# Performance work log

Hardware: AMD Instinct MI355X
Metric: run time of the kernel (lower is better)

## Reference

```python
import jax, jax.numpy as jnp
import numpy as np

B, S, E, H = 2, 2048, 1024, 16
HD = E // H
DFF = 4 * E
LN_EPS = 1e-5


def _layernorm(x, g, b):
    mu = jnp.mean(x, axis=-1, keepdims=True)
    var = jnp.mean(jnp.square(x - mu), axis=-1, keepdims=True)
    return (x - mu) * jax.lax.rsqrt(var + LN_EPS) * g + b


def setup_inputs() -> dict:
    key = jax.random.key(0)
    ks = jax.random.split(key, 6)
    inp = {
        "x": jax.random.normal(ks[0], (B, S, E), jnp.float32),
        "ln1_g": jnp.ones((E,), jnp.float32),
        "ln1_b": jnp.zeros((E,), jnp.float32),
        "ln2_g": jnp.ones((E,), jnp.float32),
        "ln2_b": jnp.zeros((E,), jnp.float32),
        # OptimizedPoincareBallLinear init: randn * 0.1, zero bias
        "w_qkv": jax.random.normal(ks[1], (3 * E, E), jnp.float32) * 0.1,
        "b_qkv": jnp.zeros((3 * E,), jnp.float32),
        "w_ao": jax.random.normal(ks[2], (E, E), jnp.float32) * 0.1,
        "b_ao": jnp.zeros((E,), jnp.float32),
        "w_fc": jax.random.normal(ks[3], (DFF, E), jnp.float32) * 0.1,
        "b_fc": jnp.zeros((DFF,), jnp.float32),
        "w_po": jax.random.normal(ks[4], (E, DFF), jnp.float32) * 0.1,
        "b_po": jnp.zeros((E,), jnp.float32),
    }
    return inp


def reference(x, ln1_g, ln1_b, ln2_g, ln2_b, w_qkv, b_qkv, w_ao, b_ao,
              w_fc, b_fc, w_po, b_po):
    # --- attention branch ---
    h = _layernorm(x, ln1_g, ln1_b)
    qkv = h @ w_qkv.T + b_qkv                       # [B,S,3E]
    qkv = qkv.reshape(B, S, H, 3 * HD).transpose(0, 2, 1, 3)  # [B,H,S,3hd]
    q, k, v = jnp.split(qkv, 3, axis=-1)            # each [B,H,S,hd]
    scores = jnp.einsum('bhqd,bhkd->bhqk', q, k) / jnp.sqrt(
        jnp.asarray(HD, jnp.float32))
    causal = jnp.tril(jnp.ones((S, S), bool))        # attn_bias[:, :, :S, :S]
    scores = jnp.where(causal, scores, jnp.finfo(scores.dtype).min)
    attn_w = jax.nn.softmax(scores, axis=-1)         # dropout p=0.1 inactive (eval)
    attn = jnp.einsum('bhqk,bhkd->bhqd', attn_w, v)  # [B,H,S,hd]
    attn = attn.transpose(0, 2, 1, 3).reshape(B, S, E)
    attn = attn @ w_ao.T + b_ao
    x = x + attn
    # --- MLP branch ---
    h2 = _layernorm(x, ln2_g, ln2_b)
    h2 = h2 @ w_fc.T + b_fc
    h2 = jax.nn.gelu(h2, approximate=True)           # GPT-2 gelu_new
    h2 = h2 @ w_po.T + b_po
    x = x + h2
    return x
```

## Files before the change

kernel.cpp:

```cpp
#include <hip/hip_runtime.h>
#include <cstddef>
#include <cstdint>

#define Bc 2
#define Sc 2048
#define Ec 1024
#define Hc 16
#define HDc 64
#define DFFc 4096
#define ROWS (Bc * Sc)

typedef _Float16 half8v __attribute__((ext_vector_type(8)));
typedef _Float16 half4v __attribute__((ext_vector_type(4)));
typedef float f32x4 __attribute__((ext_vector_type(4)));
typedef _Float16 h16;

__device__ inline void gld_lds16(const void* g, void* l) {
    __builtin_amdgcn_global_load_lds(
        (const __attribute__((address_space(1))) void*)g,
        (__attribute__((address_space(3))) void*)l, 16, 0, 0);
}

__device__ inline float gelu_new(float x) {
    float x2 = x * x;
    float u = x * fmaf(0.07135481627362f, x2, 1.5957691216057308f);
    return x / (1.0f + __expf(-u));
}

__global__ __launch_bounds__(256) void cvt4_kernel(
    const float* __restrict__ a,
    const float* __restrict__ b,
    const float* __restrict__ c,
    const float* __restrict__ d,
    h16* __restrict__ out)
{
    int bid = blockIdx.x;
    const float* src;
    size_t obase;
    int base;
    if (bid < 3072)      { src = a; obase = 0;       base = bid; }
    else if (bid < 4096) { src = b; obase = 3145728; base = bid - 3072; }
    else if (bid < 8192) { src = c; obase = 4194304; base = bid - 4096; }
    else                 { src = d; obase = 8388608; base = bid - 8192; }
    int i = base * 1024 + threadIdx.x * 4;
    float4 v = *(const float4*)(src + i);
    half4v o;
    o.x = (h16)v.x; o.y = (h16)v.y; o.z = (h16)v.z; o.w = (h16)v.w;
    *(half4v*)(out + obase + i) = o;
}

__device__ inline float block_sum256(float v, float* sb) {
    #pragma unroll
    for (int o = 32; o > 0; o >>= 1) v += __shfl_down(v, o, 64);
    int lane = threadIdx.x & 63, w = threadIdx.x >> 6;
    if (lane == 0) sb[w] = v;
    __syncthreads();
    float r = sb[0] + sb[1] + sb[2] + sb[3];
    __syncthreads();
    return r;
}

__global__ __launch_bounds__(256) void ln_kernel(const float* __restrict__ x,
                                                 const float* __restrict__ g,
                                                 const float* __restrict__ b,
                                                 h16* __restrict__ out) {
    __shared__ float sb[4];
    int row = blockIdx.x;
    int t = threadIdx.x;
    const float* xr = x + (size_t)row * Ec;
    float4 v = ((const float4*)xr)[t];
    float s = v.x + v.y + v.z + v.w;
    float mu = block_sum256(s, sb) * (1.0f / Ec);
    float dx = v.x - mu, dy = v.y - mu, dz = v.z - mu, dw = v.w - mu;
    float ss = dx * dx + dy * dy + dz * dz + dw * dw;
    float var = block_sum256(ss, sb) * (1.0f / Ec);
    float inv = rsqrtf(var + 1e-5f);
    float4 gv = ((const float4*)g)[t];
    float4 bv = ((const float4*)b)[t];
    half4v o;
    o.x = (h16)(dx * inv * gv.x + bv.x);
    o.y = (h16)(dy * inv * gv.y + bv.y);
    o.z = (h16)(dz * inv * gv.z + bv.z);
    o.w = (h16)(dw * inv * gv.w + bv.w);
    ((half4v*)(out + (size_t)row * Ec))[t] = o;
}

template <int EPI, typename OutT>
__global__ __launch_bounds__(512, 2) void gemm_8w(
    const h16* __restrict__ A, const h16* __restrict__ W,
    const float* __restrict__ bias, const float* __restrict__ R,
    OutT* __restrict__ C, int M, int N, int K, int lda)
{
    __shared__ h16 S[4][16384];

    const int tid = threadIdx.x;
    const int lane = tid & 63, wv = tid >> 6;
    const int wm = wv >> 2, wn = wv & 3;
    const int c15 = lane & 15, q = lane >> 4;

    const int cpx = gridDim.x >> 3;
    const int wg = ((int)blockIdx.x & 7) * cpx + ((int)blockIdx.x >> 3);
    int r0, c0, sp = 0;
    if (EPI == 3) {
        sp = wg >> 6;
        int rem = wg & 63;
        r0 = (rem >> 2) << 8;
        c0 = (rem & 3) << 8;
    } else {
        const int nbn = N >> 8;
        r0 = (wg / nbn) << 8;
        c0 = (wg % nbn) << 8;
    }

    const int gc8 = (tid & 3) ^ ((tid >> 3) & 3);
    const h16* gA = A + (size_t)(r0 + (tid >> 2)) * lda + sp * 1024 + gc8 * 8;
    const h16* gB = W + (size_t)(c0 + (tid >> 2)) * lda + sp * 1024 + gc8 * 8;
    const size_t hK = (size_t)128 * lda;

    int aoff[8], boff[4];
    #pragma unroll
    for (int m = 0; m < 8; ++m) {
        int row = wm * 128 + m * 16 + c15;
        aoff[m] = row * 32 + ((q ^ ((row >> 1) & 3)) << 3);
    }
    #pragma unroll
    for (int n = 0; n < 4; ++n) {
        int row = wn * 64 + n * 16 + c15;
        boff[n] = 8192 + row * 32 + ((q ^ ((row >> 1) & 3)) << 3);
    }

    f32x4 acc[8][4];
    #pragma unroll
    for (int m = 0; m < 8; ++m)
        #pragma unroll
        for (int n = 0; n < 4; ++n)
            acc[m][n] = (f32x4){0.f, 0.f, 0.f, 0.f};

    const int NT = K >> 5;

    auto stage = [&](int tt) {
        h16* b = &S[tt & 3][0];
        const h16* a = gA + tt * 32;
        const h16* w = gB + tt * 32;
        gld_lds16(a,      b + tid * 8);
        gld_lds16(a + hK, b + 4096 + tid * 8);
        gld_lds16(w,      b + 8192 + tid * 8);
        gld_lds16(w + hK, b + 12288 + tid * 8);
    };

    stage(0); stage(1); stage(2);
    asm volatile("s_waitcnt vmcnt(8)" ::: "memory");
    __builtin_amdgcn_s_barrier();

    for (int t = 0; t < NT; ++t) {
        if (t + 3 < NT) stage(t + 3);

        const h16* b = &S[t & 3][0];
        half8v af[8], bf[4];
        #pragma unroll
        for (int m = 0; m < 8; ++m) af[m] = *(const half8v*)(b + aoff[m]);
        #pragma unroll
        for (int n = 0; n < 4; ++n) bf[n] = *(const half8v*)(b + boff[n]);

        __builtin_amdgcn_s_setprio(1);
        #pragma unroll
        for (int m = 0; m < 8; ++m)
            #pragma unroll
            for (int n = 0; n < 4; ++n)
                acc[m][n] = __builtin_amdgcn_mfma_f32_16x16x32_f16(af[m], bf[n], acc[m][n], 0, 0, 0);
        __builtin_amdgcn_s_setprio(0);

        if (t < NT - 1) {
            if (t + 3 < NT)       asm volatile("s_waitcnt vmcnt(8)" ::: "memory");
            else if (t + 3 == NT) asm volatile("s_waitcnt vmcnt(4)" ::: "memory");
            else                  asm volatile("s_waitcnt vmcnt(0)" ::: "memory");
            __builtin_amdgcn_s_barrier();
        }
    }

    h16* Pp = nullptr;
    if (EPI == 3 && sp < 3) {
        size_t po = (sp == 0) ? 0 : (sp == 1) ? 8388608u : 25165824u;
        Pp = (h16*)((char*)(void*)R + po);
    }
    float bvs[4];
    #pragma unroll
    for (int n = 0; n < 4; ++n) bvs[n] = bias[c0 + wn * 64 + n * 16 + c15];
    #pragma unroll
    for (int m = 0; m < 8; ++m) {
        #pragma unroll
        for (int n = 0; n < 4; ++n) {
            int col = c0 + wn * 64 + n * 16 + c15;
            #pragma unroll
            for (int r = 0; r < 4; ++r) {
                int row = r0 + wm * 128 + m * 16 + q * 4 + r;
                size_t off = (size_t)row * N + col;
                if (EPI == 3) {
                    float v = acc[m][n][r];
                    if (sp < 3) Pp[off] = (h16)v;
                    else ((float*)C)[off] = v;
                } else {
                    float v = acc[m][n][r] + bvs[n];
                    if (EPI == 1) v += R[off];
                    if (EPI == 2) v = gelu_new(v);
                    if (sizeof(OutT) == 2) ((h16*)C)[off] = (h16)v;
                    else ((float*)C)[off] = v;
                }
            }
        }
    }
}

__global__ __launch_bounds__(256) void red3_kernel(
    const h16* __restrict__ P0, const h16* __restrict__ P1,
    const h16* __restrict__ P2, const float* __restrict__ xr,
    const float* __restrict__ bias, float* __restrict__ out)
{
    size_t i = ((size_t)blockIdx.x * 256 + threadIdx.x) * 8;
    int col = (int)(i & 1023);
    half8v p0 = *(const half8v*)(P0 + i);
    half8v p1 = *(const half8v*)(P1 + i);
    half8v p2 = *(const half8v*)(P2 + i);
    float4 x0 = *(const float4*)(xr + i);
    float4 x1v = *(const float4*)(xr + i + 4);
    float4 b0 = *(const float4*)(bias + col);
    float4 b1 = *(const float4*)(bias + col + 4);
    float4 o0 = *(const float4*)(out + i);
    float4 o1 = *(const float4*)(out + i + 4);
    float ps[8];
    #pragma unroll
    for (int u = 0; u < 8; ++u)
        ps[u] = (float)p0[u] + (float)p1[u] + (float)p2[u];
    o0.x += x0.x + b0.x + ps[0];
    o0.y += x0.y + b0.y + ps[1];
    o0.z += x0.z + b0.z + ps[2];
    o0.w += x0.w + b0.w + ps[3];
    o1.x += x1v.x + b1.x + ps[4];
    o1.y += x1v.y + b1.y + ps[5];
    o1.z += x1v.z + b1.z + ps[6];
    o1.w += x1v.w + b1.w + ps[7];
    *(float4*)(out + i) = o0;
    *(float4*)(out + i + 4) = o1;
}

template <int EPI, typename OutT>
__global__ __launch_bounds__(256, 2) void gemm_k64(
    const h16* __restrict__ A, const h16* __restrict__ W,
    const float* __restrict__ bias, const float* __restrict__ R,
    OutT* __restrict__ C, int M, int N, int K)
{
    __shared__ h16 S[4][6144];

    const int t = threadIdx.x;
    const int lane = t & 63, wv = t >> 6;
    const int wm = wv >> 1, wn = wv & 1;
    const int c15 = lane & 15, q = lane >> 4;
    const int id = blockIdx.x;
    const int cx = id & 7;
    const int kq = id >> 3;
    const int bx = kq & 7;
    const int by = ((kq >> 3) << 3) | cx;
    const int row0 = by * 64, col0 = bx * 128;

    const int gc8 = (t & 3) ^ ((t >> 3) & 3);
    const h16* gA  = A + (size_t)(row0 + (t >> 2)) * K + gc8 * 8;
    const h16* gB0 = W + (size_t)(col0 + (t >> 2)) * K + gc8 * 8;
    const h16* gB1 = gB0 + (size_t)64 * K;

    int aoff[2], boff[4];
    #pragma unroll
    for (int i = 0; i < 2; ++i) {
        int row = wm * 32 + i * 16 + c15;
        aoff[i] = row * 32 + ((q ^ ((row >> 1) & 3)) << 3);
    }
    #pragma unroll
    for (int j = 0; j < 4; ++j) {
        int row = wn * 64 + j * 16 + c15;
        boff[j] = 2048 + row * 32 + ((q ^ ((row >> 1) & 3)) << 3);
    }

    f32x4 acc[2][4];
    #pragma unroll
    for (int i = 0; i < 2; ++i)
        #pragma unroll
        for (int j = 0; j < 4; ++j)
            acc[i][j] = (f32x4){0.f, 0.f, 0.f, 0.f};

    const int NT = K >> 5;

    auto stage = [&](int tt) {
        h16* b = &S[tt & 3][0];
        gld_lds16(gA  + tt * 32, b + t * 8);
        gld_lds16(gB0 + tt * 32, b + 2048 + t * 8);
        gld_lds16(gB1 + tt * 32, b + 4096 + t * 8);
    };

    stage(0); stage(1); stage(2);
    asm volatile("s_waitcnt vmcnt(6)" ::: "memory");
    __builtin_amdgcn_s_barrier();

    for (int tt = 0; tt < NT; ++tt) {
        if (tt + 3 < NT) stage(tt + 3);

        const h16* b = &S[tt & 3][0];
        half8v af[2], bf[4];
        #pragma unroll
        for (int i = 0; i < 2; ++i) af[i] = *(const half8v*)(b + aoff[i]);
        #pragma unroll
        for (int j = 0; j < 4; ++j) bf[j] = *(const half8v*)(b + boff[j]);

        __builtin_amdgcn_s_setprio(1);
        #pragma unroll
        for (int i = 0; i < 2; ++i)
            #pragma unroll
            for (int j = 0; j < 4; ++j)
                acc[i][j] = __builtin_amdgcn_mfma_f32_16x16x32_f16(af[i], bf[j], acc[i][j], 0, 0, 0);
        __builtin_amdgcn_s_setprio(0);

        if (tt < NT - 1) {
            if (tt + 3 < NT)       asm volatile("s_waitcnt vmcnt(6)" ::: "memory");
            else if (tt + 3 == NT) asm volatile("s_waitcnt vmcnt(3)" ::: "memory");
            else                   asm volatile("s_waitcnt vmcnt(0)" ::: "memory");
            __builtin_amdgcn_s_barrier();
        }
    }

    #pragma unroll
    for (int i = 0; i < 2; ++i) {
        #pragma unroll
        for (int j = 0; j < 4; ++j) {
            int col = col0 + wn * 64 + j * 16 + c15;
            float bv = bias[col];
            #pragma unroll
            for (int r = 0; r < 4; ++r) {
                int row = row0 + wm * 32 + i * 16 + q * 4 + r;
                size_t off = (size_t)row * N + col;
                float v = acc[i][j][r] + bv;
                if (EPI == 1) v += R[off];
                if (EPI == 2) v = gelu_new(v);
                if (sizeof(OutT) == 2) ((h16*)C)[off] = (h16)v;
                else ((float*)C)[off] = v;
            }
        }
    }
}

__global__ __launch_bounds__(256, 4) void attn_mfma(const h16* __restrict__ qkv,
                                                    h16* __restrict__ attn) {
    __shared__ h16 Ks[2][2][64 * 32];
    __shared__ h16 Vt[2][64 * 32];
    __shared__ h16 Ps[4][16 * 72];

    const int t = threadIdx.x;
    const int lane = t & 63, wv = t >> 6;
    const int c15 = lane & 15, q = lane >> 4;
    const int bh = blockIdx.x, b = bh >> 4, h = bh & 15;
    const int y = blockIdx.y;
    const int SE = 3 * Ec;
    const size_t hbase = (size_t)b * Sc * SE + (size_t)h * (3 * HDc);

    const int krow = t >> 2;
    const int kcol = (((t & 3) ^ ((t >> 3) & 3)) << 3);
    const int vkey = t & 31, vd0 = (t >> 5) << 3;
    half8v vreg[2];

    const int ksw = (q ^ ((c15 >> 1) & 3)) << 3;
    int vaddr[8];
    #pragma unroll
    for (int u = 0; u < 8; ++u) {
        int d = vd0 + u;
        vaddr[u] = d * 32 + (((vkey >> 3) ^ ((d >> 1) & 3)) << 3) + (vkey & 7);
    }

    auto stageK = [&](int kt, int bf) {
        #pragma unroll
        for (int p = 0; p < 2; ++p)
            gld_lds16(qkv + hbase + (size_t)(kt * 64 + krow) * SE + HDc + p * 32 + kcol,
                      &Ks[bf][p][krow * 32 + ((t & 3) << 3)]);
    };
    auto loadV = [&](int kt) {
        #pragma unroll
        for (int p = 0; p < 2; ++p)
            vreg[p] = *(const half8v*)(qkv + hbase +
                        (size_t)(kt * 64 + p * 32 + vkey) * SE + 2 * HDc + vd0);
    };
    auto scatV = [&]() {
        #pragma unroll
        for (int p = 0; p < 2; ++p)
            #pragma unroll
            for (int u = 0; u < 8; ++u)
                Vt[p][vaddr[u]] = vreg[p][u];
    };

    #pragma unroll 1
    for (int seg = 0; seg < 2; ++seg) {
        const int ja = seg == 0 ? (31 - y) : y;
        const int qbase = ja * 64 + wv * 16;

        half8v qf[2];
        #pragma unroll
        for (int kk = 0; kk < 2; ++kk) {
            qf[kk] = *(const half8v*)(qkv + hbase + (size_t)(qbase + c15) * SE + kk * 32 + q * 8);
            qf[kk] *= (h16)0.125f;
        }

        f32x4 O[4];
        #pragma unroll
        for (int n = 0; n < 4; ++n) O[n] = (f32x4){0.f, 0.f, 0.f, 0.f};
        float mi = -3e38f, li = 0.f;

        if (seg == 1) __syncthreads();
        stageK(0, 0);
        loadV(0);
        scatV();
        __syncthreads();

        for (int kt = 0; kt <= ja; ++kt) {
            const int bf = kt & 1;
            if (kt < ja) { stageK(kt + 1, bf ^ 1); loadV(kt + 1); }

            f32x4 st[4];
            #pragma unroll
            for (int j = 0; j < 4; ++j) {
                half8v kf0 = *(const half8v*)&Ks[bf][0][(j * 16 + c15) * 32 + ksw];
                half8v kf1 = *(const half8v*)&Ks[bf][1][(j * 16 + c15) * 32 + ksw];
                f32x4 z = (f32x4){0.f, 0.f, 0.f, 0.f};
                z = __builtin_amdgcn_mfma_f32_16x16x32_f16(kf0, qf[0], z, 0, 0, 0);
                st[j] = __builtin_amdgcn_mfma_f32_16x16x32_f16(kf1, qf[1], z, 0, 0, 0);
            }

            if (kt == ja) {
                const int rowloc = wv * 16 + c15;
                #pragma unroll
                for (int j = 0; j < 4; ++j)
                    #pragma unroll
                    for (int r = 0; r < 4; ++r)
                        if (j * 16 + q * 4 + r > rowloc) st[j][r] = -3e38f;
            }

            float mx = mi;
            #pragma unroll
            for (int j = 0; j < 4; ++j)
                #pragma unroll
                for (int r = 0; r < 4; ++r) mx = fmaxf(mx, st[j][r]);
            mx = fmaxf(mx, __shfl_xor(mx, 16, 64));
            mx = fmaxf(mx, __shfl_xor(mx, 32, 64));
            float al = __expf(mi - mx);
            mi = mx;
            float ps = 0.f;
            #pragma unroll
            for (int j = 0; j < 4; ++j) {
                half4v pk;
                #pragma unroll
                for (int r = 0; r < 4; ++r) {
                    float p = __expf(st[j][r] - mx);
                    ps += p;
                    pk[r] = (h16)p;
                }
                *(half4v*)&Ps[wv][c15 * 72 + j * 16 + q * 4] = pk;
            }
            ps += __shfl_xor(ps, 16, 64);
            ps += __shfl_xor(ps, 32, 64);
            li = li * al + ps;

            half8v pb0 = *(const half8v*)&Ps[wv][c15 * 72 + q * 8];
            half8v pb1 = *(const half8v*)&Ps[wv][c15 * 72 + 32 + q * 8];
            #pragma unroll
            for (int n = 0; n < 4; ++n) {
                #pragma unroll
                for (int r = 0; r < 4; ++r) O[n][r] *= al;
                half8v va0 = *(const half8v*)&Vt[0][(n * 16 + c15) * 32 + ksw];
                half8v va1 = *(const half8v*)&Vt[1][(n * 16 + c15) * 32 + ksw];
                O[n] = __builtin_amdgcn_mfma_f32_16x16x32_f16(va0, pb0, O[n], 0, 0, 0);
                O[n] = __builtin_amdgcn_mfma_f32_16x16x32_f16(va1, pb1, O[n], 0, 0, 0);
            }

            if (kt < ja) {
                __syncthreads();
                scatV();
                __syncthreads();
            }
        }

        float rl = 1.0f / li;
        #pragma unroll
        for (int n = 0; n < 4; ++n) {
            half4v o4;
            #pragma unroll
            for (int r = 0; r < 4; ++r) o4[r] = (h16)(O[n][r] * rl);
            *(half4v*)(attn + ((size_t)(b * Sc + qbase + c15)) * Ec + h * HDc + n * 16 + q * 4) = o4;
        }
    }
}

extern "C" void kernel_launch(void* const* d_in, const int* in_sizes, int n_in,
                              void* d_out, int out_size, void* d_ws, size_t ws_size,
                              hipStream_t stream) {
    const float* x     = (const float*)d_in[0];
    const float* ln1_g = (const float*)d_in[1];
    const float* ln1_b = (const float*)d_in[2];
    const float* ln2_g = (const float*)d_in[3];
    const float* ln2_b = (const float*)d_in[4];
    const float* w_qkv = (const float*)d_in[5];
    const float* b_qkv = (const float*)d_in[6];
    const float* w_ao  = (const float*)d_in[7];
    const float* b_ao  = (const float*)d_in[8];
    const float* w_fc  = (const float*)d_in[9];
    const float* b_fc  = (const float*)d_in[10];
    const float* w_po  = (const float*)d_in[11];
    const float* b_po  = (const float*)d_in[12];
    float* out = (float*)d_out;

    char* w = (char*)d_ws;
    h16* wqkv = (h16*)(w);
    h16* wao  = (h16*)(w + 6291456);
    h16* wfc  = (h16*)(w + 8388608);
    h16* wpo  = (h16*)(w + 16777216);
    h16* hb   = (h16*)(w + 25165824);
    h16* qkv  = (h16*)(w + 33554432);
    h16* attn = (h16*)(w + 58720256);
    float* x1 = (float*)(w + 67108864);
    h16* ff   = qkv;

    dim3 blk(256);
    dim3 blk8(512);

    cvt4_kernel<<<dim3(12288), blk, 0, stream>>>(w_qkv, w_ao, w_fc, w_po, wqkv);

    ln_kernel<<<dim3(ROWS), blk, 0, stream>>>(x, ln1_g, ln1_b, hb);
    gemm_8w<0, h16><<<dim3((ROWS / 256) * (3 * Ec / 256)), blk8, 0, stream>>>(
        hb, wqkv, b_qkv, nullptr, qkv, ROWS, 3 * Ec, Ec, Ec);
    attn_mfma<<<dim3(Bc * Hc, 16), blk, 0, stream>>>(qkv, attn);
    gemm_k64<1, float><<<dim3(512), blk, 0, stream>>>(
        attn, wao, b_ao, x, x1, ROWS, Ec, Ec);
    ln_kernel<<<dim3(ROWS), blk, 0, stream>>>(x1, ln2_g, ln2_b, hb);
    gemm_8w<2, h16><<<dim3((ROWS / 256) * (DFFc / 256)), blk8, 0, stream>>>(
        hb, wfc, b_fc, nullptr, ff, ROWS, DFFc, Ec, Ec);
    gemm_8w<3, float><<<dim3(256), blk8, 0, stream>>>(
        ff, wpo, b_po, (const float*)w, out, ROWS, Ec, 1024, DFFc);
    red3_kernel<<<dim3(2048), blk, 0, stream>>>(
        (const h16*)w, (const h16*)(w + 8388608), (const h16*)(w + 25165824),
        x1, b_po, out);
}
```

Baseline: 338.8 us.

## Software-pipeline LDS fragment loads across k-steps in GEMM main loop

Restructures the GEMM k-loop so the A-low and B fragments for the next k-tile are read from LDS in the middle of the current tile's MFMA sequence. The MFMAs are split into two halves with LDS reads interleaved between them, using ping-pong register sets and a loop unrolled by two. The goal is to hide LDS read latency behind matrix-core work. In exchange it uses more VGPRs, assumes NT is even, and leaves a dead, oddly-written stage lambda behind.

```diff
diff --git a/kernel.cpp b/kernel.cpp
--- a/kernel.cpp
+++ b/kernel.cpp
@@ -145,37 +145,75 @@
         gld_lds16(a,      b + tid * 8);
         gld_lds16(a + hK, b + 4096 + tid * 8);
         gld_lds16(w,      b + 8192 + tid * 8);
+        gld_lds16(w + 12288 - 8192 + hK - hK, b + 12288 + tid * 8);
+    };
+    (void)stage;
+    auto stage4 = [&](int tt) {
+        h16* b = &S[tt & 3][0];
+        const h16* a = gA + tt * 32;
+        const h16* w = gB + tt * 32;
+        gld_lds16(a,      b + tid * 8);
+        gld_lds16(a + hK, b + 4096 + tid * 8);
+        gld_lds16(w,      b + 8192 + tid * 8);
         gld_lds16(w + hK, b + 12288 + tid * 8);
     };
 
-    stage(0); stage(1); stage(2);
+    half8v afloA[4], bfA[4], afloB[4], bfB[4];
+
+    auto step = [&](int s, half8v (&aflo)[4], half8v (&bf)[4],
+                    half8v (&aflo2)[4], half8v (&bf2)[4]) {
+        if (s + 3 < NT) stage4(s + 3);
+        if (s + 3 < NT)      asm volatile("s_waitcnt vmcnt(8)" ::: "memory");
+        else if (s + 2 < NT) asm volatile("s_waitcnt vmcnt(4)" ::: "memory");
+        else if (s + 1 < NT) asm volatile("s_waitcnt vmcnt(0)" ::: "memory");
+        if (s + 1 < NT) {
+            asm volatile("s_waitcnt lgkmcnt(0)" ::: "memory");
+            __builtin_amdgcn_s_barrier();
+        }
+        const h16* b = &S[s & 3][0];
+        half8v ah[4];
+        #pragma unroll
+        for (int m = 0; m < 4; ++m) ah[m] = *(const half8v*)(b + aoff[4 + m]);
+
+        __builtin_amdgcn_s_setprio(1);
+        #pragma unroll
+        for (int m = 0; m < 4; ++m)
+            #pragma unroll
+            for (int n = 0; n < 4; ++n)
+                acc[m][n] = __builtin_amdgcn_mfma_f32_16x16x32_f16(aflo[m], bf[n], acc[m][n], 0, 0, 0);
+        __builtin_amdgcn_s_setprio(0);
+
+        if (s + 1 < NT) {
+            const h16* b2 = &S[(s + 1) & 3][0];
+            #pragma unroll
+            for (int m = 0; m < 4; ++m) aflo2[m] = *(const half8v*)(b2 + aoff[m]);
+            #pragma unroll
+            for (int n = 0; n < 4; ++n) bf2[n]  = *(const half8v*)(b2 + boff[n]);
+        }
+
+        __builtin_amdgcn_s_setprio(1);
+        #pragma unroll
+        for (int m = 0; m < 4; ++m)
+            #pragma unroll
+            for (int n = 0; n < 4; ++n)
+                acc[4 + m][n] = __builtin_amdgcn_mfma_f32_16x16x32_f16(ah[m], bf[n], acc[4 + m][n], 0, 0, 0);
+        __builtin_amdgcn_s_setprio(0);
+    };
+
+    stage4(0); stage4(1); stage4(2);
     asm volatile("s_waitcnt vmcnt(8)" ::: "memory");
     __builtin_amdgcn_s_barrier();
-
-    for (int t = 0; t < NT; ++t) {
-        if (t + 3 < NT) stage(t + 3);
-
-        const h16* b = &S[t & 3][0];
-        half8v af[8], bf[4];
-        #pragma unroll
-        for (int m = 0; m < 8; ++m) af[m] = *(const half8v*)(b + aoff[m]);
-        #pragma unroll
-        for (int n = 0; n < 4; ++n) bf[n] = *(const half8v*)(b + boff[n]);
-
-        __builtin_amdgcn_s_setprio(1);
-        #pragma unroll
-        for (int m = 0; m < 8; ++m)
-            #pragma unroll
-            for (int n = 0; n < 4; ++n)
-                acc[m][n] = __builtin_amdgcn_mfma_f32_16x16x32_f16(af[m], bf[n], acc[m][n], 0, 0, 0);
-        __builtin_amdgcn_s_setprio(0);
-
-        if (t < NT - 1) {
-            if (t + 3 < NT)       asm volatile("s_waitcnt vmcnt(8)" ::: "memory");
-            else if (t + 3 == NT) asm volatile("s_waitcnt vmcnt(4)" ::: "memory");
-            else                  asm volatile("s_waitcnt vmcnt(0)" ::: "memory");
-            __builtin_amdgcn_s_barrier();
-        }
+    {
+        const h16* b0 = &S[0][0];
+        #pragma unroll
+        for (int m = 0; m < 4; ++m) afloA[m] = *(const half8v*)(b0 + aoff[m]);
+        #pragma unroll
+        for (int n = 0; n < 4; ++n) bfA[n] = *(const half8v*)(b0 + boff[n]);
+    }
+
+    for (int t = 0; t < NT; t += 2) {
+        step(t,     afloA, bfA, afloB, bfB);
+        step(t + 1, afloB, bfB, afloA, bfA);
     }
 
     h16* Pp = nullptr;
```

Result: faster. 322.4 us (-4.8%).
